# Performance work log

Measured on AMD Instinct MI355X. Metric: run time of the kernel, lower is better.

The kernel has to match this reference:

```python
import jax, jax.numpy as jnp
import numpy as np


def setup_inputs() -> dict:
    key = jax.random.key(0)
    k0, k1, k2, k3 = jax.random.split(key, 4)
    B, S, E, D, L = 4, 128, 768, 128, 40
    return {
        "emb0": jax.random.normal(k0, (B, S, E), jnp.float32),
        "emb1": jax.random.normal(k1, (B, S, E), jnp.float32),
        "att": jnp.ones((B, S), dtype=bool),
        "W_arc": jax.random.normal(k2, (D, E), jnp.float32) * 0.05,
        "W_lbl": jax.random.normal(k3, (L, 2 * E), jnp.float32) * 0.05,
    }


def reference(emb0, emb1, att, W_arc, W_lbl):
    B, S, E = emb1.shape
    L = W_lbl.shape[0]
    # --- RootedGraphPredictor: linear transform + all-pairs squared distances ---
    dep = jnp.einsum('bse,de->bsd', emb0, W_arc)                      # [B,S,D]
    diff = dep[:, :, None, :] - dep[:, None, :, :]                    # [B,S,S,D]
    distances = jnp.sum(diff * diff, axis=-1)                         # [B,S,S]
    # log(softmin(distances)) == log_softmax(-distances)
    parent = jax.nn.log_softmax(-distances, axis=-1)                  # [B,S,S]
    # --- DependencyLabelClassifier ---
    # Faithful packing order of emb_sentences_expanded: first S*(S-1) rows are
    # (i,j) pairs in row-major order SKIPPING the diagonal, last S rows are
    # (emb[i], ones). The attention mask, however, is laid out in FULL row-major
    # (j,k) order (index j*S+k) -- this mismatch is in the original code and is
    # reproduced faithfully here.
    p = jnp.arange(S * S)
    tail = p >= S * (S - 1)
    i_comp = p // (S - 1)
    j_raw = p % (S - 1)
    j_comp = j_raw + (j_raw >= i_comp).astype(j_raw.dtype)
    i_idx = jnp.where(tail, p - S * (S - 1), i_comp)
    j_idx = jnp.where(tail, 0, j_comp)
    first = emb1[:, i_idx, :]                                          # [B,S*S,E]
    second = jnp.where(tail[None, :, None], 1.0, emb1[:, j_idx, :])    # [B,S*S,E]
    pair = jnp.concatenate([first, second], axis=-1)                   # [B,S*S,2E]
    mlp_out = jnp.einsum('bpe,le->bpl', pair, W_lbl)                   # [B,S*S,L]
    eye = jnp.eye(S, dtype=bool)
    mask = (att[:, :, None] & att[:, None, :] & ~eye).reshape(B, S * S)
    logits = jnp.where(mask[:, :, None], mlp_out, -jnp.inf)            # [B,S*S,L]
    lbl_logits = jnp.log(logits).reshape(B, S, S, L)                   # log of logits (nan where <=0/-inf)
    lbl_parent = jnp.nan_to_num(lbl_logits + parent[:, :, :, None], nan=-10.0)
    return (dep, distances, lbl_parent)
```

## Files before the change

### kernel.cpp

```cpp
#include <hip/hip_runtime.h>


__device__ __forceinline__ float wsum_f32(float v) {
#pragma unroll
    for (int off = 32; off; off >>= 1) v += __shfl_down(v, off, 64);
    return v;
}
__device__ __forceinline__ double wsum_f64(double v) {
#pragma unroll
    for (int off = 32; off; off >>= 1) v += __shfl_down(v, off, 64);
    return v;
}

__global__ __launch_bounds__(256) void k1_proj(
    const float* __restrict__ emb0,
    const float* __restrict__ emb1,
    const float* __restrict__ W_arc,
    const float* __restrict__ W_lbl,
    float* __restrict__ out_dep,
    double* __restrict__ A1,
    double* __restrict__ A2,
    double* __restrict__ Cd)
{
    const int tid  = threadIdx.x;
    const int lane = tid & 63;
    const int wv   = tid >> 6;
    const int blk  = blockIdx.x;
    const int base = lane * 4;

    if (blk < 256) {
        __shared__ float e0[1536];
        __shared__ float col_out[256];
        const int r0 = blk * 2;
        const float* src = emb0 + r0 * 768;
        for (int idx = tid * 4; idx < 1536; idx += 1024)
            *(float4*)(e0 + idx) = *(const float4*)(src + idx);
        __syncthreads();

        const float4 ea0 = *(const float4*)(e0 + base);
        const float4 ea1 = *(const float4*)(e0 + 256 + base);
        const float4 ea2 = *(const float4*)(e0 + 512 + base);
        const float4 eb0 = *(const float4*)(e0 + 768 + base);
        const float4 eb1 = *(const float4*)(e0 + 1024 + base);
        const float4 eb2 = *(const float4*)(e0 + 1280 + base);

        for (int cc = 0; cc < 32; ++cc) {
            const int c = wv * 32 + cc;
            const float* w = W_arc + c * 768 + base;
            const float4 w0 = *(const float4*)(w);
            const float4 w1 = *(const float4*)(w + 256);
            const float4 w2 = *(const float4*)(w + 512);
            float s0 = w0.x*ea0.x + w0.y*ea0.y + w0.z*ea0.z + w0.w*ea0.w
                     + w1.x*ea1.x + w1.y*ea1.y + w1.z*ea1.z + w1.w*ea1.w
                     + w2.x*ea2.x + w2.y*ea2.y + w2.z*ea2.z + w2.w*ea2.w;
            float s1 = w0.x*eb0.x + w0.y*eb0.y + w0.z*eb0.z + w0.w*eb0.w
                     + w1.x*eb1.x + w1.y*eb1.y + w1.z*eb1.z + w1.w*eb1.w
                     + w2.x*eb2.x + w2.y*eb2.y + w2.z*eb2.z + w2.w*eb2.w;
            s0 = wsum_f32(s0);
            s1 = wsum_f32(s1);
            if (lane == 0) { col_out[c] = s0; col_out[128 + c] = s1; }
        }
        __syncthreads();
        out_dep[r0 * 128 + tid] = col_out[tid];
    } else {
        __shared__ float e1[1536];
        __shared__ double a_out[160];
        const int r0 = (blk - 256) * 2;
        const float* src = emb1 + r0 * 768;
        for (int idx = tid * 4; idx < 1536; idx += 1024)
            *(float4*)(e1 + idx) = *(const float4*)(src + idx);
        __syncthreads();

        const float4 fa0 = *(const float4*)(e1 + base);
        const float4 fa1 = *(const float4*)(e1 + 256 + base);
        const float4 fa2 = *(const float4*)(e1 + 512 + base);
        const float4 fb0 = *(const float4*)(e1 + 768 + base);
        const float4 fb1 = *(const float4*)(e1 + 1024 + base);
        const float4 fb2 = *(const float4*)(e1 + 1280 + base);

        for (int cc = 0; cc < 20; ++cc) {
            const int col  = wv * 20 + cc;
            const int half = col / 40;
            const int l    = col - half * 40;
            const float* w = W_lbl + l * 1536 + half * 768 + base;
            const float4 w0 = *(const float4*)(w);
            const float4 w1 = *(const float4*)(w + 256);
            const float4 w2 = *(const float4*)(w + 512);
            double s0 = (double)w0.x*fa0.x + (double)w0.y*fa0.y + (double)w0.z*fa0.z + (double)w0.w*fa0.w
                      + (double)w1.x*fa1.x + (double)w1.y*fa1.y + (double)w1.z*fa1.z + (double)w1.w*fa1.w
                      + (double)w2.x*fa2.x + (double)w2.y*fa2.y + (double)w2.z*fa2.z + (double)w2.w*fa2.w;
            double s1 = (double)w0.x*fb0.x + (double)w0.y*fb0.y + (double)w0.z*fb0.z + (double)w0.w*fb0.w
                      + (double)w1.x*fb1.x + (double)w1.y*fb1.y + (double)w1.z*fb1.z + (double)w1.w*fb1.w
                      + (double)w2.x*fb2.x + (double)w2.y*fb2.y + (double)w2.z*fb2.z + (double)w2.w*fb2.w;
            s0 = wsum_f64(s0);
            s1 = wsum_f64(s1);
            if (lane == 0) { a_out[col] = s0; a_out[80 + col] = s1; }
        }
        __syncthreads();
        if (tid < 160) {
            const int row = tid / 80, rem = tid - row * 80;
            const int half = rem / 40, l = rem - half * 40;
            double* dst = half ? A2 : A1;
            dst[(r0 + row) * 40 + l] = a_out[row * 80 + rem];
        }
        if (blk == 256) {
            for (int cc = 0; cc < 10; ++cc) {
                const int l = wv * 10 + cc;
                const float* w = W_lbl + l * 1536 + 768 + base;
                const float4 w0 = *(const float4*)(w);
                const float4 w1 = *(const float4*)(w + 256);
                const float4 w2 = *(const float4*)(w + 512);
                double s = (double)w0.x + (double)w0.y + (double)w0.z + (double)w0.w
                         + (double)w1.x + (double)w1.y + (double)w1.z + (double)w1.w
                         + (double)w2.x + (double)w2.y + (double)w2.z + (double)w2.w;
                s = wsum_f64(s);
                if (lane == 0) Cd[l] = s;
            }
        }
    }
}

__global__ __launch_bounds__(256) void k2_rows(
    const float* __restrict__ dep,
    const double* __restrict__ A1,
    const double* __restrict__ A2,
    const double* __restrict__ Cd,
    float* __restrict__ out_dist,
    float* __restrict__ out_lbl)
{
    __shared__ float depi[128];
    __shared__ float dists[128];
    __shared__ float red[2];
    __shared__ float lse_sh;

    const int tid = threadIdx.x;
    const int bi = blockIdx.x;
    const int b = bi >> 7;
    const int i = bi & 127;
    const float* depb = dep + b * (128 * 128);

    if (tid < 128) depi[tid] = depb[i * 128 + tid];
    __syncthreads();

    float ex = 0.0f;
    if (tid < 128) {
        const int j = tid;
        const float* dj = depb + j * 128;
        float acc = 0.0f;
        for (int d = 0; d < 128; d += 4) {
            float4 v = *(const float4*)(dj + d);
            float d0 = v.x - depi[d + 0];
            float d1 = v.y - depi[d + 1];
            float d2 = v.z - depi[d + 2];
            float d3 = v.w - depi[d + 3];
            acc += d0 * d0 + d1 * d1 + d2 * d2 + d3 * d3;
        }
        dists[j] = acc;
        out_dist[bi * 128 + j] = acc;
        ex = expf(-acc);
    }

    float sum = ex;
#pragma unroll
    for (int off = 32; off >= 1; off >>= 1) sum += __shfl_down(sum, off, 64);
    if (tid < 128 && (tid & 63) == 0) red[tid >> 6] = sum;
    __syncthreads();
    if (tid == 0) lse_sh = logf(red[0] + red[1]);
    __syncthreads();

    const float lse = lse_sh;
    const bool last = (i == 127);
    const double* A1b = A1 + b * (128 * 40);
    const double* A2b = A2 + b * (128 * 40);
    float* outrow = out_lbl + bi * 5120;

    if (!last) {
        const double* a1row0 = A1b + i * 40;
        const double* a1row1 = A1b + (i + 1) * 40;
        for (int k = 0; k < 5; ++k) {
            const int idx = k * 1024 + tid * 4;
            float4 o;
            float* oc = &o.x;
#pragma unroll
            for (int e = 0; e < 4; ++e) {
                const int id = idx + e;
                const int j = id / 40;
                const int l = id - j * 40;
                float r;
                if (j == i) {
                    r = -10.0f;
                } else {
                    const int s2 = i + j;
                    const int carry = (s2 >= 127) ? 1 : 0;
                    const int jr = s2 - 127 * carry;
                    const int jm = jr + ((jr >= i + carry) ? 1 : 0);
                    const double v = (carry ? a1row1[l] : a1row0[l]) + A2b[jm * 40 + l];
                    r = (v > 0.0) ? (logf((float)v) - dists[j] - lse)
                      : ((v < 0.0) ? -10.0f : -3.4028234663852886e+38f);
                }
                oc[e] = r;
            }
            *(float4*)(outrow + idx) = o;
        }
    } else {
        for (int k = 0; k < 5; ++k) {
            const int idx = k * 1024 + tid * 4;
            float4 o;
            float* oc = &o.x;
#pragma unroll
            for (int e = 0; e < 4; ++e) {
                const int id = idx + e;
                const int j = id / 40;
                const int l = id - j * 40;
                float r;
                if (j == i) {
                    r = -10.0f;
                } else {
                    const double v = A1b[j * 40 + l] + Cd[l];
                    r = (v > 0.0) ? (logf((float)v) - dists[j] - lse)
                      : ((v < 0.0) ? -10.0f : -3.4028234663852886e+38f);
                }
                oc[e] = r;
            }
            *(float4*)(outrow + idx) = o;
        }
    }
}

extern "C" void kernel_launch(void* const* d_in, const int* in_sizes, int n_in,
                              void* d_out, int out_size, void* d_ws, size_t ws_size,
                              hipStream_t stream)
{
    const float* emb0  = (const float*)d_in[0];
    const float* emb1  = (const float*)d_in[1];
    const float* W_arc = (const float*)d_in[3];
    const float* W_lbl = (const float*)d_in[4];

    float* out      = (float*)d_out;
    float* out_dep  = out;
    float* out_dist = out + 65536;
    float* out_lbl  = out + 131072;

    char* ws = (char*)d_ws;
    double* A1 = (double*)(ws);
    double* A2 = (double*)(ws + 163840);
    double* Cd = (double*)(ws + 327680);

    hipLaunchKernelGGL(k1_proj, dim3(512), dim3(256), 0, stream,
                       emb0, emb1, W_arc, W_lbl, out_dep, A1, A2, Cd);
    hipLaunchKernelGGL(k2_rows, dim3(512), dim3(256), 0, stream,
                       out_dep, A1, A2, Cd, out_dist, out_lbl);
}
```

Measured before the change: 96.37 us.

## Split projection kernel: partial-sum reductions, one row per label block, prefetch weights

In the arc projection, the full 6-step wavefront reduction is replaced by two xor shuffles plus a shared-memory partial-sum buffer, which a second pass reduces per output. The label projection now processes one emb1 row per block (512 blocks instead of 256), software-prefetches the next weight column, and writes A1/A2 directly without a shared staging buffer. The constant Cd reduction moves to its own dedicated block. The aim is to shorten the serial shuffle chains and raise parallelism for the double-precision path, at the cost of more blocks each reloading the W_lbl slices.

```diff
diff --git a/kernel.cpp b/kernel.cpp
--- a/kernel.cpp
+++ b/kernel.cpp
@@ -1,11 +1,6 @@
 #include <hip/hip_runtime.h>
 
 
-__device__ __forceinline__ float wsum_f32(float v) {
-#pragma unroll
-    for (int off = 32; off; off >>= 1) v += __shfl_down(v, off, 64);
-    return v;
-}
 __device__ __forceinline__ double wsum_f64(double v) {
 #pragma unroll
     for (int off = 32; off; off >>= 1) v += __shfl_down(v, off, 64);
@@ -30,7 +25,7 @@
 
     if (blk < 256) {
         __shared__ float e0[1536];
-        __shared__ float col_out[256];
+        __shared__ float pd[2 * 128 * 17];
         const int r0 = blk * 2;
         const float* src = emb0 + r0 * 768;
         for (int idx = tid * 4; idx < 1536; idx += 1024)
@@ -50,72 +45,77 @@
             const float4 w0 = *(const float4*)(w);
             const float4 w1 = *(const float4*)(w + 256);
             const float4 w2 = *(const float4*)(w + 512);
-            float s0 = w0.x*ea0.x + w0.y*ea0.y + w0.z*ea0.z + w0.w*ea0.w
+            float p0 = w0.x*ea0.x + w0.y*ea0.y + w0.z*ea0.z + w0.w*ea0.w
                      + w1.x*ea1.x + w1.y*ea1.y + w1.z*ea1.z + w1.w*ea1.w
                      + w2.x*ea2.x + w2.y*ea2.y + w2.z*ea2.z + w2.w*ea2.w;
-            float s1 = w0.x*eb0.x + w0.y*eb0.y + w0.z*eb0.z + w0.w*eb0.w
+            float p1 = w0.x*eb0.x + w0.y*eb0.y + w0.z*eb0.z + w0.w*eb0.w
                      + w1.x*eb1.x + w1.y*eb1.y + w1.z*eb1.z + w1.w*eb1.w
                      + w2.x*eb2.x + w2.y*eb2.y + w2.z*eb2.z + w2.w*eb2.w;
-            s0 = wsum_f32(s0);
-            s1 = wsum_f32(s1);
-            if (lane == 0) { col_out[c] = s0; col_out[128 + c] = s1; }
+            p0 += __shfl_xor(p0, 16, 64);  p0 += __shfl_xor(p0, 32, 64);
+            p1 += __shfl_xor(p1, 16, 64);  p1 += __shfl_xor(p1, 32, 64);
+            if (lane < 16) {
+                pd[c * 17 + lane]            = p0;
+                pd[128 * 17 + c * 17 + lane] = p1;
+            }
         }
         __syncthreads();
-        out_dep[r0 * 128 + tid] = col_out[tid];
-    } else {
-        __shared__ float e1[1536];
-        __shared__ double a_out[160];
-        const int r0 = (blk - 256) * 2;
-        const float* src = emb1 + r0 * 768;
-        for (int idx = tid * 4; idx < 1536; idx += 1024)
-            *(float4*)(e1 + idx) = *(const float4*)(src + idx);
+        {
+            const int row = tid >> 7, col = tid & 127;
+            const float* p = pd + row * (128 * 17) + col * 17;
+            float s = 0.f;
+#pragma unroll
+            for (int q = 0; q < 16; ++q) s += p[q];
+            out_dep[(r0 + row) * 128 + col] = s;
+        }
+    } else if (blk < 768) {
+        __shared__ float e1[768];
+        const int row = blk - 256;
+        const float* src = emb1 + row * 768;
+        if (tid * 4 < 768)
+            *(float4*)(e1 + tid * 4) = *(const float4*)(src + tid * 4);
         __syncthreads();
 
         const float4 fa0 = *(const float4*)(e1 + base);
         const float4 fa1 = *(const float4*)(e1 + 256 + base);
         const float4 fa2 = *(const float4*)(e1 + 512 + base);
-        const float4 fb0 = *(const float4*)(e1 + 768 + base);
-        const float4 fb1 = *(const float4*)(e1 + 1024 + base);
-        const float4 fb2 = *(const float4*)(e1 + 1280 + base);
-
+
+        int col = wv * 20;
+        const float* w = W_lbl + (col % 40) * 1536 + (col / 40) * 768 + base;
+        float4 w0 = *(const float4*)(w);
+        float4 w1 = *(const float4*)(w + 256);
+        float4 w2 = *(const float4*)(w + 512);
         for (int cc = 0; cc < 20; ++cc) {
-            const int col  = wv * 20 + cc;
-            const int half = col / 40;
-            const int l    = col - half * 40;
-            const float* w = W_lbl + l * 1536 + half * 768 + base;
+            float4 n0, n1, n2;
+            if (cc < 19) {
+                const int nc = col + 1;
+                const float* nw = W_lbl + (nc % 40) * 1536 + (nc / 40) * 768 + base;
+                n0 = *(const float4*)(nw);
+                n1 = *(const float4*)(nw + 256);
+                n2 = *(const float4*)(nw + 512);
+            }
+            double s = (double)w0.x*fa0.x + (double)w0.y*fa0.y + (double)w0.z*fa0.z + (double)w0.w*fa0.w
+                     + (double)w1.x*fa1.x + (double)w1.y*fa1.y + (double)w1.z*fa1.z + (double)w1.w*fa1.w
+                     + (double)w2.x*fa2.x + (double)w2.y*fa2.y + (double)w2.z*fa2.z + (double)w2.w*fa2.w;
+            s = wsum_f64(s);
+            if (lane == 0) {
+                const int half = col / 40, l = col - half * 40;
+                (half ? A2 : A1)[row * 40 + l] = s;
+            }
+            col += 1;
+            w0 = n0; w1 = n1; w2 = n2;
+        }
+    } else {
+        for (int cc = 0; cc < 10; ++cc) {
+            const int l = wv * 10 + cc;
+            const float* w = W_lbl + l * 1536 + 768 + base;
             const float4 w0 = *(const float4*)(w);
             const float4 w1 = *(const float4*)(w + 256);
             const float4 w2 = *(const float4*)(w + 512);
-            double s0 = (double)w0.x*fa0.x + (double)w0.y*fa0.y + (double)w0.z*fa0.z + (double)w0.w*fa0.w
-                      + (double)w1.x*fa1.x + (double)w1.y*fa1.y + (double)w1.z*fa1.z + (double)w1.w*fa1.w
-                      + (double)w2.x*fa2.x + (double)w2.y*fa2.y + (double)w2.z*fa2.z + (double)w2.w*fa2.w;
-            double s1 = (double)w0.x*fb0.x + (double)w0.y*fb0.y + (double)w0.z*fb0.z + (double)w0.w*fb0.w
-                      + (double)w1.x*fb1.x + (double)w1.y*fb1.y + (double)w1.z*fb1.z + (double)w1.w*fb1.w
-                      + (double)w2.x*fb2.x + (double)w2.y*fb2.y + (double)w2.z*fb2.z + (double)w2.w*fb2.w;
-            s0 = wsum_f64(s0);
-            s1 = wsum_f64(s1);
-            if (lane == 0) { a_out[col] = s0; a_out[80 + col] = s1; }
-        }
-        __syncthreads();
-        if (tid < 160) {
-            const int row = tid / 80, rem = tid - row * 80;
-            const int half = rem / 40, l = rem - half * 40;
-            double* dst = half ? A2 : A1;
-            dst[(r0 + row) * 40 + l] = a_out[row * 80 + rem];
-        }
-        if (blk == 256) {
-            for (int cc = 0; cc < 10; ++cc) {
-                const int l = wv * 10 + cc;
-                const float* w = W_lbl + l * 1536 + 768 + base;
-                const float4 w0 = *(const float4*)(w);
-                const float4 w1 = *(const float4*)(w + 256);
-                const float4 w2 = *(const float4*)(w + 512);
-                double s = (double)w0.x + (double)w0.y + (double)w0.z + (double)w0.w
-                         + (double)w1.x + (double)w1.y + (double)w1.z + (double)w1.w
-                         + (double)w2.x + (double)w2.y + (double)w2.z + (double)w2.w;
-                s = wsum_f64(s);
-                if (lane == 0) Cd[l] = s;
-            }
+            double s = (double)w0.x + (double)w0.y + (double)w0.z + (double)w0.w
+                     + (double)w1.x + (double)w1.y + (double)w1.z + (double)w1.w
+                     + (double)w2.x + (double)w2.y + (double)w2.z + (double)w2.w;
+            s = wsum_f64(s);
+            if (lane == 0) Cd[l] = s;
         }
     }
 }
@@ -246,7 +246,7 @@
     double* A2 = (double*)(ws + 163840);
     double* Cd = (double*)(ws + 327680);
 
-    hipLaunchKernelGGL(k1_proj, dim3(512), dim3(256), 0, stream,
+    hipLaunchKernelGGL(k1_proj, dim3(769), dim3(256), 0, stream,
                        emb0, emb1, W_arc, W_lbl, out_dep, A1, A2, Cd);
     hipLaunchKernelGGL(k2_rows, dim3(512), dim3(256), 0, stream,
                        out_dep, A1, A2, Cd, out_dist, out_lbl);
```

After: 93.65 us. 2.8% less time.
